# Performance work log

Measured on AMD Instinct MI355X. Metric: run time of the kernel, lower is better.

Reference implementation:

```python
import jax, jax.numpy as jnp
import numpy as np

B, F, C, H, W = 2, 16, 320, 32, 32
HEADS, DH, G = 8, 40, 32
INNER = 4 * C  # GEGLU hidden = 1280
MAXLEN = 25


def make_pe(maxlen, dm):
    pos = np.arange(maxlen)[:, None].astype(np.float64)
    div = np.exp(np.arange(0, dm, 2) * (-np.log(10000.0) / dm))
    pe = np.zeros((maxlen, dm), np.float32)
    pe[:, 0::2] = np.sin(pos * div)
    pe[:, 1::2] = np.cos(pos * div)
    return jnp.asarray(pe)

PE = make_pe(MAXLEN, C)  # [max_len, C], constant buffer


def layernorm(x, g, b, eps=1e-5):
    m = x.mean(-1, keepdims=True)
    v = jnp.var(x, axis=-1, keepdims=True)
    return (x - m) * jax.lax.rsqrt(v + eps) * g + b


def temporal_attn(hs, f, wq, wk, wv, wo, bo):
    # hs: [(b*f), d, c]; rearrange '(b f) d c -> (b d) f c'
    bf, d, c = hs.shape
    bb = bf // f
    t = hs.reshape(bb, f, d, c).transpose(0, 2, 1, 3).reshape(bb * d, f, c)
    t = t + PE[:f]  # temporal positional encoding
    def split_heads(y):
        return y.reshape(bb * d, f, HEADS, DH).transpose(0, 2, 1, 3)  # [n,h,f,dh]
    q = split_heads(t @ wq)
    k = split_heads(t @ wk)
    v = split_heads(t @ wv)
    scores = jnp.einsum('nhqd,nhkd->nhqk', q, k) * (DH ** -0.5)  # fp32
    probs = jax.nn.softmax(scores, axis=-1)
    o = jnp.einsum('nhqk,nhkd->nhqd', probs, v)
    o = o.transpose(0, 2, 1, 3).reshape(bb * d, f, c)
    o = o @ wo + bo
    # rearrange '(b d) f c -> (b f) d c'
    return o.reshape(bb, d, f, c).transpose(0, 2, 1, 3).reshape(bf, d, c)


def setup_inputs() -> dict:
    key = jax.random.key(0)
    ks = iter(jax.random.split(key, 40))
    def p(shape, s=0.02):
        return jax.random.normal(next(ks), shape, jnp.float32) * s
    inp = {"x": jax.random.normal(next(ks), (B, F, C, H, W), jnp.float32)}
    inp["gn_w"] = jnp.ones((C,), jnp.float32); inp["gn_b"] = jnp.zeros((C,), jnp.float32)
    inp["pin_w"] = p((C, C)); inp["pin_b"] = jnp.zeros((C,), jnp.float32)
    for i in (1, 2):
        inp[f"ln{i}_w"] = jnp.ones((C,), jnp.float32); inp[f"ln{i}_b"] = jnp.zeros((C,), jnp.float32)
        inp[f"wq{i}"] = p((C, C)); inp[f"wk{i}"] = p((C, C)); inp[f"wv{i}"] = p((C, C))
        inp[f"wo{i}"] = p((C, C)); inp[f"bo{i}"] = jnp.zeros((C,), jnp.float32)
    inp["ffln_w"] = jnp.ones((C,), jnp.float32); inp["ffln_b"] = jnp.zeros((C,), jnp.float32)
    inp["ff_w1"] = p((C, 2 * INNER)); inp["ff_b1"] = jnp.zeros((2 * INNER,), jnp.float32)
    inp["ff_w2"] = p((INNER, C)); inp["ff_b2"] = jnp.zeros((C,), jnp.float32)
    inp["pout_w"] = p((C, C)); inp["pout_b"] = jnp.zeros((C,), jnp.float32)
    return inp


def reference(x, gn_w, gn_b, pin_w, pin_b,
              ln1_w, ln1_b, wq1, wk1, wv1, wo1, bo1,
              ln2_w, ln2_b, wq2, wk2, wv2, wo2, bo2,
              ffln_w, ffln_b, ff_w1, ff_b1, ff_w2, ff_b2,
              pout_w, pout_b):
    b, f, c, h, w = x.shape
    xf = x.reshape(b * f, c, h, w)
    residual = xf
    # GroupNorm(32, eps=1e-6)
    xg = xf.reshape(b * f, G, c // G, h * w)
    m = xg.mean((2, 3), keepdims=True)
    v = jnp.var(xg, axis=(2, 3), keepdims=True)
    xg = (xg - m) * jax.lax.rsqrt(v + 1e-6)
    xn = xg.reshape(b * f, c, h, w) * gn_w[:, None, None] + gn_b[:, None, None]
    # to tokens + proj_in
    hs = xn.transpose(0, 2, 3, 1).reshape(b * f, h * w, c)
    hs = hs @ pin_w + pin_b
    # TemporalTransformerBlock: two temporal self-attn blocks + GEGLU FF
    hs = hs + temporal_attn(layernorm(hs, ln1_w, ln1_b), f, wq1, wk1, wv1, wo1, bo1)
    hs = hs + temporal_attn(layernorm(hs, ln2_w, ln2_b), f, wq2, wk2, wv2, wo2, bo2)
    y = layernorm(hs, ffln_w, ffln_b) @ ff_w1 + ff_b1
    a, gate = jnp.split(y, 2, axis=-1)
    hs = hs + ((a * jax.nn.gelu(gate, approximate=False)) @ ff_w2 + ff_b2)
    # proj_out + spatial residual
    hs = hs @ pout_w + pout_b
    out = hs.reshape(b * f, h, w, c).transpose(0, 3, 1, 2) + residual
    return out.reshape(b, f, c, h, w)
```

## Files before the change

### kernel.cpp

```cpp
#include <hip/hip_runtime.h>
#include <hip/hip_bf16.h>
#include <math.h>

typedef __hip_bfloat16 bf16;
typedef __attribute__((ext_vector_type(8))) short bf16x8;
typedef __attribute__((ext_vector_type(4))) float f32x4;

#define NT    32768
#define CH    320
#define NSEQ  2048
#define FRAMES 16
#define HEADS 8
#define DHEAD 40
#define INNER 1280
#define HW    1024
#define NIMG  32

__device__ __forceinline__ float b2f(bf16 v) { return __bfloat162float(v); }
__device__ __forceinline__ bf16  f2b(float v) { return __float2bfloat16(v); }
__device__ __forceinline__ float bfbits2f(unsigned short u) {
  union { unsigned int i; float f; } x; x.i = ((unsigned int)u) << 16; return x.f;
}
__device__ __forceinline__ unsigned short f2bfbits(float f) {
  union { float f; unsigned int i; } x; x.f = f;
  return (unsigned short)((x.i + 0x7FFF + ((x.i >> 16) & 1)) >> 16);
}

__device__ __forceinline__ void stage16(const bf16* g, bf16* l) {
  __builtin_amdgcn_global_load_lds(
      (const __attribute__((address_space(1))) void*)g,
      (__attribute__((address_space(3))) void*)l, 16, 0, 0);
}

__device__ __forceinline__ float block_reduce_sum(float v, float* sbuf) {
  int lane = threadIdx.x & 63;
  int wv   = threadIdx.x >> 6;
#pragma unroll
  for (int off = 32; off; off >>= 1) v += __shfl_down(v, off);
  __syncthreads();
  if (lane == 0) sbuf[wv] = v;
  __syncthreads();
  int nw = ((int)blockDim.x + 63) >> 6;
  float r = 0.f;
  for (int i = 0; i < nw; ++i) r += sbuf[i];
  return r;
}

struct TD { const float* src; bf16* dst; int K, N, t0; };
struct TDs { TD d[12]; };
__global__ __launch_bounds__(256) void transpose_w_kernel(TDs td, int ndesc) {
  __shared__ float tile[32][33];
  int bt = blockIdx.x;
  int mi = 0;
  for (int i = 1; i < 12; ++i) if (i < ndesc && bt >= td.d[i].t0) mi = i;
  TD e = td.d[mi];
  int lt = bt - e.t0;
  int ntx = e.N >> 5;
  int kt = lt / ntx, nt = lt - kt * ntx;
#pragma unroll
  for (int q = 0; q < 4; ++q) {
    int idx = threadIdx.x + q * 256; int r = idx >> 5, c = idx & 31;
    tile[r][c] = e.src[(size_t)(kt * 32 + r) * e.N + nt * 32 + c];
  }
  __syncthreads();
#pragma unroll
  for (int q = 0; q < 4; ++q) {
    int idx = threadIdx.x + q * 256; int r = idx >> 5, c = idx & 31;
    e.dst[(size_t)(nt * 32 + r) * e.K + kt * 32 + c] = f2b(tile[c][r]);
  }
}

__global__ __launch_bounds__(256) void pe_table_kernel(float* __restrict__ petab) {
  int i = blockIdx.x * 256 + threadIdx.x;
  if (i < 16 * CH) {
    int fi = i / CH, c = i - fi * CH;
    float arg = (float)fi * expf((float)(c & ~1) * -0.028782313662425575f);
    petab[i] = (c & 1) ? cosf(arg) : sinf(arg);
  }
}

__global__ __launch_bounds__(256) void ln_fused_kernel(const bf16* __restrict__ in,
                                                       const float* __restrict__ w,
                                                       const float* __restrict__ b,
                                                       bf16* __restrict__ out,
                                                       const float* __restrict__ petab,
                                                       int mode) {
  int wv = threadIdx.x >> 6, lane = threadIdx.x & 63;
  int row = blockIdx.x * 4 + wv;
  size_t base = (size_t)row * CH;
  float v[5];
  float s = 0.f;
#pragma unroll
  for (int j = 0; j < 5; ++j) {
    v[j] = b2f(in[base + lane + 64 * j]);
    s += v[j];
  }
#pragma unroll
  for (int off = 32; off; off >>= 1) s += __shfl_down(s, off);
  float mean = __shfl(s, 0) * (1.f / 320.f);
  float s2 = 0.f;
#pragma unroll
  for (int j = 0; j < 5; ++j) { float d = v[j] - mean; s2 += d * d; }
#pragma unroll
  for (int off = 32; off; off >>= 1) s2 += __shfl_down(s2, off);
  float rstd = rsqrtf(__shfl(s2, 0) * (1.f / 320.f) + 1e-5f);
  size_t obase = base;
  const float* pe = nullptr;
  if (mode) {
    int img = row >> 10, dd = row & 1023, bb = img >> 4, fi = img & 15;
    int trow = (((bb << 10) + dd) << 4) + fi;
    obase = (size_t)trow * CH;
    pe = petab + fi * CH;
  }
#pragma unroll
  for (int j = 0; j < 5; ++j) {
    int c = lane + 64 * j;
    float o = (v[j] - mean) * rstd * w[c] + b[c];
    if (mode) o += pe[c];
    out[obase + c] = f2b(o);
  }
}

__global__ __launch_bounds__(256) void gemm_mfma_kernel(
    const bf16* __restrict__ A, const bf16* __restrict__ BT,
    const float* __restrict__ bias, const bf16* res,
    bf16* C0, bf16* C1, bf16* C2, int M, int K, int rowmap) {
  __shared__ __align__(16) bf16 sA[128 * 64];
  __shared__ __align__(16) bf16 sB[64 * 64];
  int tid = threadIdx.x, lane = tid & 63, w = tid >> 6;
  int wm = w >> 1, wn = w & 1;
  int m0 = blockIdx.x * 128, n0 = blockIdx.y * 64;
  int which = n0 / 320;
  int ncol0 = n0 - which * 320;
  bf16* C = which == 0 ? C0 : (which == 1 ? C1 : C2);
  f32x4 acc[4][2];
#pragma unroll
  for (int i = 0; i < 4; ++i)
#pragma unroll
    for (int j = 0; j < 2; ++j) acc[i][j] = (f32x4){0.f, 0.f, 0.f, 0.f};

  int lr = lane >> 3;
  int cg = (lane & 7) ^ lr;
  for (int k0 = 0; k0 < K; k0 += 64) {
#pragma unroll
    for (int s = 0; s < 4; ++s) {
      int tA = w * 4 + s;
      int row = tA * 8 + lr;
      stage16(A + (size_t)(m0 + row) * K + k0 + cg * 8, sA + tA * 512);
    }
#pragma unroll
    for (int s = 0; s < 2; ++s) {
      int tB = w * 2 + s;
      int row = tB * 8 + lr;
      stage16(BT + (size_t)(n0 + row) * K + k0 + cg * 8, sB + tB * 512);
    }
    __syncthreads();
#pragma unroll
    for (int kk = 0; kk < 2; ++kk) {
      bf16x8 a[4], b[2];
      int cc = kk * 4 + (lane >> 4);
#pragma unroll
      for (int i = 0; i < 4; ++i) {
        int r = wm * 64 + i * 16 + (lane & 15);
        a[i] = *(const bf16x8*)(sA + r * 64 + ((cc ^ (r & 7)) * 8));
      }
#pragma unroll
      for (int j = 0; j < 2; ++j) {
        int n = wn * 32 + j * 16 + (lane & 15);
        b[j] = *(const bf16x8*)(sB + n * 64 + ((cc ^ (n & 7)) * 8));
      }
#pragma unroll
      for (int i = 0; i < 4; ++i)
#pragma unroll
        for (int j = 0; j < 2; ++j)
          acc[i][j] = __builtin_amdgcn_mfma_f32_16x16x32_bf16(a[i], b[j], acc[i][j], 0, 0, 0);
    }
    __syncthreads();
  }
#pragma unroll
  for (int i = 0; i < 4; ++i)
#pragma unroll
    for (int j = 0; j < 2; ++j) {
      int row0 = m0 + wm * 64 + i * 16 + (lane >> 4) * 4;
      int col  = ncol0 + wn * 32 + j * 16 + (lane & 15);
      float bv = bias ? bias[col] : 0.f;
#pragma unroll
      for (int rg = 0; rg < 4; ++rg) {
        int r = row0 + rg;
        if (rowmap) {
          int n = r >> 4, fi = r & 15, bb = n >> 10, dd = n & 1023;
          r = ((bb << 4) + fi) * 1024 + dd;
        }
        size_t idx = (size_t)r * 320 + col;
        float v = acc[i][j][rg] + bv;
        if (res) v += b2f(res[idx]);
        C[idx] = f2b(v);
      }
    }
}

__global__ __launch_bounds__(256) void gemm_mfma_geglu_kernel(
    const bf16* __restrict__ A, const bf16* __restrict__ BT,
    const float* __restrict__ b1, bf16* __restrict__ act, int M, int K) {
  __shared__ __align__(16) bf16 sA[128 * 64];
  __shared__ __align__(16) bf16 sBa[64 * 64];
  __shared__ __align__(16) bf16 sBg[64 * 64];
  int tid = threadIdx.x, lane = tid & 63, w = tid >> 6;
  int wm = w >> 1, wn = w & 1;
  int m0 = blockIdx.x * 128, n0 = blockIdx.y * 64;
  f32x4 aa[4][2], ag[4][2];
#pragma unroll
  for (int i = 0; i < 4; ++i)
#pragma unroll
    for (int j = 0; j < 2; ++j) {
      aa[i][j] = (f32x4){0.f, 0.f, 0.f, 0.f};
      ag[i][j] = (f32x4){0.f, 0.f, 0.f, 0.f};
    }
  int lr = lane >> 3;
  int cg = (lane & 7) ^ lr;
  for (int k0 = 0; k0 < K; k0 += 64) {
#pragma unroll
    for (int s = 0; s < 4; ++s) {
      int tA = w * 4 + s;
      int row = tA * 8 + lr;
      stage16(A + (size_t)(m0 + row) * K + k0 + cg * 8, sA + tA * 512);
    }
#pragma unroll
    for (int s = 0; s < 2; ++s) {
      int tB = w * 2 + s;
      int row = tB * 8 + lr;
      stage16(BT + (size_t)(n0 + row) * K + k0 + cg * 8, sBa + tB * 512);
      stage16(BT + (size_t)(1280 + n0 + row) * K + k0 + cg * 8, sBg + tB * 512);
    }
    __syncthreads();
#pragma unroll
    for (int kk = 0; kk < 2; ++kk) {
      bf16x8 a[4], ba[2], bg[2];
      int cc = kk * 4 + (lane >> 4);
#pragma unroll
      for (int i = 0; i < 4; ++i) {
        int r = wm * 64 + i * 16 + (lane & 15);
        a[i] = *(const bf16x8*)(sA + r * 64 + ((cc ^ (r & 7)) * 8));
      }
#pragma unroll
      for (int j = 0; j < 2; ++j) {
        int n = wn * 32 + j * 16 + (lane & 15);
        ba[j] = *(const bf16x8*)(sBa + n * 64 + ((cc ^ (n & 7)) * 8));
        bg[j] = *(const bf16x8*)(sBg + n * 64 + ((cc ^ (n & 7)) * 8));
      }
#pragma unroll
      for (int i = 0; i < 4; ++i)
#pragma unroll
        for (int j = 0; j < 2; ++j) {
          aa[i][j] = __builtin_amdgcn_mfma_f32_16x16x32_bf16(a[i], ba[j], aa[i][j], 0, 0, 0);
          ag[i][j] = __builtin_amdgcn_mfma_f32_16x16x32_bf16(a[i], bg[j], ag[i][j], 0, 0, 0);
        }
    }
    __syncthreads();
  }
#pragma unroll
  for (int i = 0; i < 4; ++i)
#pragma unroll
    for (int j = 0; j < 2; ++j) {
      int row0 = m0 + wm * 64 + i * 16 + (lane >> 4) * 4;
      int col  = n0 + wn * 32 + j * 16 + (lane & 15);
      float bva = b1[col], bvg = b1[1280 + col];
#pragma unroll
      for (int rg = 0; rg < 4; ++rg) {
        float av = aa[i][j][rg] + bva;
        float gv = ag[i][j][rg] + bvg;
        float gelu = 0.5f * gv * (1.0f + erff(gv * 0.70710678118654752f));
        act[(size_t)(row0 + rg) * 1280 + col] = f2b(av * gelu);
      }
    }
}

__global__ __launch_bounds__(256) void gn_stats_kernel(const float* __restrict__ x,
                                                       float* __restrict__ stat) {
  __shared__ float sbuf[8];
  int g  = blockIdx.x;
  int im = blockIdx.y;
  const float* base = x + ((size_t)im * CH + (size_t)g * 10) * HW;
  float s = 0.f, s2 = 0.f;
  for (int i = threadIdx.x; i < 10 * HW; i += 256) {
    float v = base[i];
    s += v; s2 += v * v;
  }
  s  = block_reduce_sum(s, sbuf);
  s2 = block_reduce_sum(s2, sbuf);
  if (threadIdx.x == 0) {
    float mean = s * (1.f / 10240.f);
    float var  = s2 * (1.f / 10240.f) - mean * mean;
    stat[(im * 32 + g) * 2 + 0] = mean;
    stat[(im * 32 + g) * 2 + 1] = rsqrtf(var + 1e-6f);
  }
}

__global__ __launch_bounds__(256) void gn_apply_kernel(const float* __restrict__ x,
                                                       const float* __restrict__ gw,
                                                       const float* __restrict__ gb,
                                                       const float* __restrict__ stat,
                                                       bf16* __restrict__ xn) {
  __shared__ float tile[32][33];
  int st = blockIdx.x, ct = blockIdx.y, im = blockIdx.z;
  int c0 = ct * 32, s0 = st * 32;
  for (int t = threadIdx.x; t < 1024; t += 256) {
    int i = t >> 5, j = t & 31;
    int c = c0 + i;
    int g = c / 10;
    float mean = stat[(im * 32 + g) * 2 + 0];
    float rstd = stat[(im * 32 + g) * 2 + 1];
    tile[i][j] = (x[((size_t)(im * CH + c) << 10) + s0 + j] - mean) * rstd * gw[c] + gb[c];
  }
  __syncthreads();
  for (int t = threadIdx.x; t < 1024; t += 256) {
    int i = t >> 5, j = t & 31;
    xn[((size_t)(im * HW + s0 + i)) * CH + c0 + j] = f2b(tile[j][i]);
  }
}

#define AROW 324
__global__ __launch_bounds__(256) void attention_kernel(const bf16* __restrict__ Q,
                                                        const bf16* __restrict__ K,
                                                        const bf16* __restrict__ V,
                                                        bf16* __restrict__ O) {
  __shared__ float q[16 * AROW];
  __shared__ float k[16 * AROW];
  __shared__ float v[16 * AROW];
  __shared__ float sc[HEADS * 16 * 16];
  const float SCALE = 0.15811388300841897f;
  int tid = threadIdx.x;
  int n = blockIdx.x;
  size_t base = (size_t)n * FRAMES * CH;
  for (int j = tid; j < 1280; j += 256) {
    int row = j / 80, off = (j - row * 80) * 4;
    int src = row * 320 + off;
    ushort4 uq = *(const ushort4*)(Q + base + src);
    ushort4 uk = *(const ushort4*)(K + base + src);
    ushort4 uv = *(const ushort4*)(V + base + src);
    float* qd = &q[row * AROW + off];
    float* kd = &k[row * AROW + off];
    float* vd = &v[row * AROW + off];
    qd[0] = bfbits2f(uq.x) * SCALE; qd[1] = bfbits2f(uq.y) * SCALE;
    qd[2] = bfbits2f(uq.z) * SCALE; qd[3] = bfbits2f(uq.w) * SCALE;
    kd[0] = bfbits2f(uk.x); kd[1] = bfbits2f(uk.y);
    kd[2] = bfbits2f(uk.z); kd[3] = bfbits2f(uk.w);
    vd[0] = bfbits2f(uv.x); vd[1] = bfbits2f(uv.y);
    vd[2] = bfbits2f(uv.z); vd[3] = bfbits2f(uv.w);
  }
  __syncthreads();
  {
    int h = tid >> 5, sub = tid & 31, qf = sub >> 1, kfg = sub & 1;
    const float* qrow = &q[qf * AROW + h * DHEAD];
    float s[8] = {0.f, 0.f, 0.f, 0.f, 0.f, 0.f, 0.f, 0.f};
#pragma unroll
    for (int d4 = 0; d4 < 10; ++d4) {
      float4 qv = *(const float4*)(qrow + d4 * 4);
#pragma unroll
      for (int i = 0; i < 8; ++i) {
        const float* krow = &k[(kfg * 8 + i) * AROW + h * DHEAD];
        float4 kv = *(const float4*)(krow + d4 * 4);
        s[i] += qv.x * kv.x + qv.y * kv.y + qv.z * kv.z + qv.w * kv.w;
      }
    }
    float* dst = &sc[(h * 16 + qf) * 16 + kfg * 8];
#pragma unroll
    for (int i = 0; i < 8; ++i) dst[i] = s[i];
  }
  __syncthreads();
  if (tid < 128) {
    float* r = &sc[tid * 16];
    float mx = r[0];
#pragma unroll
    for (int i = 1; i < 16; ++i) mx = fmaxf(mx, r[i]);
    float sum = 0.f;
#pragma unroll
    for (int i = 0; i < 16; ++i) { float e = expf(r[i] - mx); r[i] = e; sum += e; }
    float inv = 1.0f / sum;
#pragma unroll
    for (int i = 0; i < 16; ++i) r[i] *= inv;
  }
  __syncthreads();
  for (int g = tid; g < 1280; g += 256) {
    int qf = g / 80, c4 = g - qf * 80;
    int h = c4 / 10;
    const float* p = &sc[(h * 16 + qf) * 16];
    float4 o = {0.f, 0.f, 0.f, 0.f};
#pragma unroll
    for (int kf = 0; kf < 16; ++kf) {
      float pv = p[kf];
      float4 vv = *(const float4*)&v[kf * AROW + c4 * 4];
      o.x += pv * vv.x; o.y += pv * vv.y; o.z += pv * vv.z; o.w += pv * vv.w;
    }
    ushort4 u;
    u.x = f2bfbits(o.x); u.y = f2bfbits(o.y);
    u.z = f2bfbits(o.z); u.w = f2bfbits(o.w);
    *(ushort4*)(O + base + qf * 320 + c4 * 4) = u;
  }
}

__global__ __launch_bounds__(256) void final_kernel(const bf16* __restrict__ proj,
                                                    const float* __restrict__ x,
                                                    float* __restrict__ out) {
  __shared__ float tile[32][33];
  int st = blockIdx.x, ct = blockIdx.y, im = blockIdx.z;
  int c0 = ct * 32, s0 = st * 32;
  for (int t = threadIdx.x; t < 1024; t += 256) {
    int i = t >> 5, j = t & 31;
    tile[i][j] = b2f(proj[((size_t)(im * HW + s0 + i)) * CH + c0 + j]);
  }
  __syncthreads();
  for (int t = threadIdx.x; t < 1024; t += 256) {
    int i = t >> 5, j = t & 31;
    size_t idx = ((size_t)(im * CH + c0 + i) << 10) + s0 + j;
    out[idx] = tile[j][i] + x[idx];
  }
}

extern "C" void kernel_launch(void* const* d_in, const int* in_sizes, int n_in,
                              void* d_out, int out_size, void* d_ws, size_t ws_size,
                              hipStream_t stream) {
  const float* x      = (const float*)d_in[0];
  const float* gn_w   = (const float*)d_in[1];
  const float* gn_b   = (const float*)d_in[2];
  const float* pin_w  = (const float*)d_in[3];
  const float* pin_b  = (const float*)d_in[4];
  const float* ffln_w = (const float*)d_in[19];
  const float* ffln_b = (const float*)d_in[20];
  const float* ff_w1  = (const float*)d_in[21];
  const float* ff_b1  = (const float*)d_in[22];
  const float* ff_w2  = (const float*)d_in[23];
  const float* ff_b2  = (const float*)d_in[24];
  const float* pout_w = (const float*)d_in[25];
  const float* pout_b = (const float*)d_in[26];

  const size_t NTC = (size_t)NT * CH;
  bf16* W0 = (bf16*)d_ws;
  bf16* W1 = W0 + NTC;
  bf16* W2 = W1 + NTC;
  bf16* W3 = W2 + NTC;
  bf16* OB = (bf16*)d_out;
  float* gnstat = (float*)d_out;
  bf16* WT = (bf16*)d_out + NTC;
  bf16* wt_pin  = WT;
  bf16* wt_qkv1 = wt_pin + 102400;
  bf16* wt_wo1  = wt_qkv1 + 307200;
  bf16* wt_qkv2 = wt_wo1 + 102400;
  bf16* wt_wo2  = wt_qkv2 + 307200;
  bf16* wt_ff1  = wt_wo2 + 102400;
  bf16* wt_ff2  = wt_ff1 + 819200;
  bf16* wt_pout = wt_ff2 + 409600;
  float* petab  = (float*)(wt_pout + 102400);

  TDs td; int t0 = 0;
  auto add = [&](int i, const float* s, bf16* d, int K, int N) {
    td.d[i] = {s, d, K, N, t0}; t0 += (K / 32) * (N / 32);
  };
  add(0, pin_w, wt_pin, 320, 320);
  add(1, (const float*)d_in[7],  wt_qkv1,          320, 320);
  add(2, (const float*)d_in[8],  wt_qkv1 + 102400, 320, 320);
  add(3, (const float*)d_in[9],  wt_qkv1 + 204800, 320, 320);
  add(4, (const float*)d_in[10], wt_wo1,           320, 320);
  add(5, (const float*)d_in[14], wt_qkv2,          320, 320);
  add(6, (const float*)d_in[15], wt_qkv2 + 102400, 320, 320);
  add(7, (const float*)d_in[16], wt_qkv2 + 204800, 320, 320);
  add(8, (const float*)d_in[17], wt_wo2,           320, 320);
  add(9, ff_w1, wt_ff1, 320, 2560);
  add(10, ff_w2, wt_ff2, 1280, 320);
  add(11, pout_w, wt_pout, 320, 320);
  transpose_w_kernel<<<t0, 256, 0, stream>>>(td, 12);
  pe_table_kernel<<<20, 256, 0, stream>>>(petab);

  dim3 g_trans(32, 10, NIMG);
  dim3 g_gemm(NT / 128, 5);

  gn_stats_kernel<<<dim3(32, NIMG), 256, 0, stream>>>(x, gnstat);
  gn_apply_kernel<<<g_trans, 256, 0, stream>>>(x, gn_w, gn_b, gnstat, W1);
  gemm_mfma_kernel<<<g_gemm, 256, 0, stream>>>(W1, wt_pin, pin_b, nullptr,
                                               W0, W0, W0, NT, CH, 0);

  for (int blk = 0; blk < 2; ++blk) {
    const float* lnw = (const float*)d_in[5 + 7 * blk];
    const float* lnb = (const float*)d_in[6 + 7 * blk];
    const float* bo  = (const float*)d_in[11 + 7 * blk];
    bf16* wt_qkv = blk ? wt_qkv2 : wt_qkv1;
    bf16* wt_wo  = blk ? wt_wo2  : wt_wo1;

    ln_fused_kernel<<<NT / 4, 256, 0, stream>>>(W0, lnw, lnb, W2, petab, 1);
    gemm_mfma_kernel<<<dim3(NT / 128, 15), 256, 0, stream>>>(W2, wt_qkv, nullptr, nullptr,
                                                             W3, OB, W1, NT, CH, 0);
    attention_kernel<<<NSEQ, 256, 0, stream>>>(W3, OB, W1, W2);
    gemm_mfma_kernel<<<g_gemm, 256, 0, stream>>>(W2, wt_wo, bo, W0,
                                                 W0, W0, W0, NT, CH, 1);
  }

  ln_fused_kernel<<<NT / 4, 256, 0, stream>>>(W0, ffln_w, ffln_b, W1, nullptr, 0);
  const int MH = NT / 2;
  for (int h = 0; h < 2; ++h) {
    const bf16* Ah = W1 + (size_t)h * MH * CH;
    bf16* act = W2;
    gemm_mfma_geglu_kernel<<<dim3(MH / 128, 20), 256, 0, stream>>>(Ah, wt_ff1, ff_b1,
                                                                   act, MH, CH);
    bf16* hsh = W0 + (size_t)h * MH * CH;
    gemm_mfma_kernel<<<dim3(MH / 128, 5), 256, 0, stream>>>(act, wt_ff2, ff_b2, hsh,
                                                            hsh, hsh, hsh, MH, INNER, 0);
  }

  gemm_mfma_kernel<<<g_gemm, 256, 0, stream>>>(W0, wt_pout, pout_b, nullptr,
                                               W1, W1, W1, NT, CH, 0);
  final_kernel<<<g_trans, 256, 0, stream>>>(W1, x, (float*)d_out);
}
```

Measured before the change: 595.7 us.

## Widen GEMM N-tiles and fuse proj_out with transpose and residual epilogue

The generic MFMA GEMM now uses 128x160 tiles instead of 128x64, and the GEGLU GEMM uses 128x128 tiles per gate/value half, so each block reuses A tiles across more columns and the grid shrinks. The proj_out GEMM gets a new rowmap==2 epilogue that writes fp32 output directly in channel-major layout and adds the input residual, which removes the separate final transpose kernel and its bf16 intermediate. The pout weight transpose moves to just before that GEMM, into a free workspace buffer. In exchange, accumulator register and LDS use per block rise, which may lower occupancy, and the fused store writes float4 along the spatial axis from MFMA row groups.

```diff
diff --git a/kernel.cpp b/kernel.cpp
--- a/kernel.cpp
+++ b/kernel.cpp
@@ -124,20 +124,22 @@
 __global__ __launch_bounds__(256) void gemm_mfma_kernel(
     const bf16* __restrict__ A, const bf16* __restrict__ BT,
     const float* __restrict__ bias, const bf16* res,
-    bf16* C0, bf16* C1, bf16* C2, int M, int K, int rowmap) {
+    bf16* C0, bf16* C1, bf16* C2,
+    const float* __restrict__ resF, float* __restrict__ outF,
+    int M, int K, int rowmap) {
   __shared__ __align__(16) bf16 sA[128 * 64];
-  __shared__ __align__(16) bf16 sB[64 * 64];
+  __shared__ __align__(16) bf16 sB[160 * 64];
   int tid = threadIdx.x, lane = tid & 63, w = tid >> 6;
   int wm = w >> 1, wn = w & 1;
-  int m0 = blockIdx.x * 128, n0 = blockIdx.y * 64;
+  int m0 = blockIdx.x * 128, n0 = blockIdx.y * 160;
   int which = n0 / 320;
   int ncol0 = n0 - which * 320;
   bf16* C = which == 0 ? C0 : (which == 1 ? C1 : C2);
-  f32x4 acc[4][2];
+  f32x4 acc[4][5];
 #pragma unroll
   for (int i = 0; i < 4; ++i)
 #pragma unroll
-    for (int j = 0; j < 2; ++j) acc[i][j] = (f32x4){0.f, 0.f, 0.f, 0.f};
+    for (int j = 0; j < 5; ++j) acc[i][j] = (f32x4){0.f, 0.f, 0.f, 0.f};
 
   int lr = lane >> 3;
   int cg = (lane & 7) ^ lr;
@@ -149,15 +151,15 @@
       stage16(A + (size_t)(m0 + row) * K + k0 + cg * 8, sA + tA * 512);
     }
 #pragma unroll
-    for (int s = 0; s < 2; ++s) {
-      int tB = w * 2 + s;
+    for (int s = 0; s < 5; ++s) {
+      int tB = w * 5 + s;
       int row = tB * 8 + lr;
       stage16(BT + (size_t)(n0 + row) * K + k0 + cg * 8, sB + tB * 512);
     }
     __syncthreads();
 #pragma unroll
     for (int kk = 0; kk < 2; ++kk) {
-      bf16x8 a[4], b[2];
+      bf16x8 a[4], b[5];
       int cc = kk * 4 + (lane >> 4);
 #pragma unroll
       for (int i = 0; i < 4; ++i) {
@@ -165,14 +167,14 @@
         a[i] = *(const bf16x8*)(sA + r * 64 + ((cc ^ (r & 7)) * 8));
       }
 #pragma unroll
-      for (int j = 0; j < 2; ++j) {
-        int n = wn * 32 + j * 16 + (lane & 15);
+      for (int j = 0; j < 5; ++j) {
+        int n = wn * 80 + j * 16 + (lane & 15);
         b[j] = *(const bf16x8*)(sB + n * 64 + ((cc ^ (n & 7)) * 8));
       }
 #pragma unroll
       for (int i = 0; i < 4; ++i)
 #pragma unroll
-        for (int j = 0; j < 2; ++j)
+        for (int j = 0; j < 5; ++j)
           acc[i][j] = __builtin_amdgcn_mfma_f32_16x16x32_bf16(a[i], b[j], acc[i][j], 0, 0, 0);
     }
     __syncthreads();
@@ -180,21 +182,33 @@
 #pragma unroll
   for (int i = 0; i < 4; ++i)
 #pragma unroll
-    for (int j = 0; j < 2; ++j) {
+    for (int j = 0; j < 5; ++j) {
       int row0 = m0 + wm * 64 + i * 16 + (lane >> 4) * 4;
-      int col  = ncol0 + wn * 32 + j * 16 + (lane & 15);
+      int col  = ncol0 + wn * 80 + j * 16 + (lane & 15);
       float bv = bias ? bias[col] : 0.f;
-#pragma unroll
-      for (int rg = 0; rg < 4; ++rg) {
-        int r = row0 + rg;
-        if (rowmap) {
-          int n = r >> 4, fi = r & 15, bb = n >> 10, dd = n & 1023;
-          r = ((bb << 4) + fi) * 1024 + dd;
+      if (rowmap == 2) {
+        int im = row0 >> 10, s0r = row0 & 1023;
+        size_t oidx = ((size_t)(im * 320 + col) << 10) + s0r;
+        float4 xr = *(const float4*)(resF + oidx);
+        float4 ov;
+        ov.x = acc[i][j][0] + bv + xr.x;
+        ov.y = acc[i][j][1] + bv + xr.y;
+        ov.z = acc[i][j][2] + bv + xr.z;
+        ov.w = acc[i][j][3] + bv + xr.w;
+        *(float4*)(outF + oidx) = ov;
+      } else {
+#pragma unroll
+        for (int rg = 0; rg < 4; ++rg) {
+          int r = row0 + rg;
+          if (rowmap == 1) {
+            int n = r >> 4, fi = r & 15, bb = n >> 10, dd = n & 1023;
+            r = ((bb << 4) + fi) * 1024 + dd;
+          }
+          size_t idx = (size_t)r * 320 + col;
+          float v = acc[i][j][rg] + bv;
+          if (res) v += b2f(res[idx]);
+          C[idx] = f2b(v);
         }
-        size_t idx = (size_t)r * 320 + col;
-        float v = acc[i][j][rg] + bv;
-        if (res) v += b2f(res[idx]);
-        C[idx] = f2b(v);
       }
     }
 }
@@ -203,16 +217,16 @@
     const bf16* __restrict__ A, const bf16* __restrict__ BT,
     const float* __restrict__ b1, bf16* __restrict__ act, int M, int K) {
   __shared__ __align__(16) bf16 sA[128 * 64];
-  __shared__ __align__(16) bf16 sBa[64 * 64];
-  __shared__ __align__(16) bf16 sBg[64 * 64];
+  __shared__ __align__(16) bf16 sBa[128 * 64];
+  __shared__ __align__(16) bf16 sBg[128 * 64];
   int tid = threadIdx.x, lane = tid & 63, w = tid >> 6;
   int wm = w >> 1, wn = w & 1;
-  int m0 = blockIdx.x * 128, n0 = blockIdx.y * 64;
-  f32x4 aa[4][2], ag[4][2];
+  int m0 = blockIdx.x * 128, n0 = blockIdx.y * 128;
+  f32x4 aa[4][4], ag[4][4];
 #pragma unroll
   for (int i = 0; i < 4; ++i)
 #pragma unroll
-    for (int j = 0; j < 2; ++j) {
+    for (int j = 0; j < 4; ++j) {
       aa[i][j] = (f32x4){0.f, 0.f, 0.f, 0.f};
       ag[i][j] = (f32x4){0.f, 0.f, 0.f, 0.f};
     }
@@ -226,8 +240,8 @@
       stage16(A + (size_t)(m0 + row) * K + k0 + cg * 8, sA + tA * 512);
     }
 #pragma unroll
-    for (int s = 0; s < 2; ++s) {
-      int tB = w * 2 + s;
+    for (int s = 0; s < 4; ++s) {
+      int tB = w * 4 + s;
       int row = tB * 8 + lr;
       stage16(BT + (size_t)(n0 + row) * K + k0 + cg * 8, sBa + tB * 512);
       stage16(BT + (size_t)(1280 + n0 + row) * K + k0 + cg * 8, sBg + tB * 512);
@@ -235,7 +249,7 @@
     __syncthreads();
 #pragma unroll
     for (int kk = 0; kk < 2; ++kk) {
-      bf16x8 a[4], ba[2], bg[2];
+      bf16x8 a[4], ba[4], bg[4];
       int cc = kk * 4 + (lane >> 4);
 #pragma unroll
       for (int i = 0; i < 4; ++i) {
@@ -243,15 +257,15 @@
         a[i] = *(const bf16x8*)(sA + r * 64 + ((cc ^ (r & 7)) * 8));
       }
 #pragma unroll
-      for (int j = 0; j < 2; ++j) {
-        int n = wn * 32 + j * 16 + (lane & 15);
+      for (int j = 0; j < 4; ++j) {
+        int n = wn * 64 + j * 16 + (lane & 15);
         ba[j] = *(const bf16x8*)(sBa + n * 64 + ((cc ^ (n & 7)) * 8));
         bg[j] = *(const bf16x8*)(sBg + n * 64 + ((cc ^ (n & 7)) * 8));
       }
 #pragma unroll
       for (int i = 0; i < 4; ++i)
 #pragma unroll
-        for (int j = 0; j < 2; ++j) {
+        for (int j = 0; j < 4; ++j) {
           aa[i][j] = __builtin_amdgcn_mfma_f32_16x16x32_bf16(a[i], ba[j], aa[i][j], 0, 0, 0);
           ag[i][j] = __builtin_amdgcn_mfma_f32_16x16x32_bf16(a[i], bg[j], ag[i][j], 0, 0, 0);
         }
@@ -261,9 +275,9 @@
 #pragma unroll
   for (int i = 0; i < 4; ++i)
 #pragma unroll
-    for (int j = 0; j < 2; ++j) {
+    for (int j = 0; j < 4; ++j) {
       int row0 = m0 + wm * 64 + i * 16 + (lane >> 4) * 4;
-      int col  = n0 + wn * 32 + j * 16 + (lane & 15);
+      int col  = n0 + wn * 64 + j * 16 + (lane & 15);
       float bva = b1[col], bvg = b1[1280 + col];
 #pragma unroll
       for (int rg = 0; rg < 4; ++rg) {
@@ -399,24 +413,6 @@
   }
 }
 
-__global__ __launch_bounds__(256) void final_kernel(const bf16* __restrict__ proj,
-                                                    const float* __restrict__ x,
-                                                    float* __restrict__ out) {
-  __shared__ float tile[32][33];
-  int st = blockIdx.x, ct = blockIdx.y, im = blockIdx.z;
-  int c0 = ct * 32, s0 = st * 32;
-  for (int t = threadIdx.x; t < 1024; t += 256) {
-    int i = t >> 5, j = t & 31;
-    tile[i][j] = b2f(proj[((size_t)(im * HW + s0 + i)) * CH + c0 + j]);
-  }
-  __syncthreads();
-  for (int t = threadIdx.x; t < 1024; t += 256) {
-    int i = t >> 5, j = t & 31;
-    size_t idx = ((size_t)(im * CH + c0 + i) << 10) + s0 + j;
-    out[idx] = tile[j][i] + x[idx];
-  }
-}
-
 extern "C" void kernel_launch(void* const* d_in, const int* in_sizes, int n_in,
                               void* d_out, int out_size, void* d_ws, size_t ws_size,
                               hipStream_t stream) {
@@ -449,8 +445,7 @@
   bf16* wt_wo2  = wt_qkv2 + 307200;
   bf16* wt_ff1  = wt_wo2 + 102400;
   bf16* wt_ff2  = wt_ff1 + 819200;
-  bf16* wt_pout = wt_ff2 + 409600;
-  float* petab  = (float*)(wt_pout + 102400);
+  float* petab  = (float*)(wt_ff2 + 409600);
 
   TDs td; int t0 = 0;
   auto add = [&](int i, const float* s, bf16* d, int K, int N) {
@@ -467,17 +462,17 @@
   add(8, (const float*)d_in[17], wt_wo2,           320, 320);
   add(9, ff_w1, wt_ff1, 320, 2560);
   add(10, ff_w2, wt_ff2, 1280, 320);
-  add(11, pout_w, wt_pout, 320, 320);
-  transpose_w_kernel<<<t0, 256, 0, stream>>>(td, 12);
+  td.d[11] = td.d[0];
+  transpose_w_kernel<<<t0, 256, 0, stream>>>(td, 11);
   pe_table_kernel<<<20, 256, 0, stream>>>(petab);
 
   dim3 g_trans(32, 10, NIMG);
-  dim3 g_gemm(NT / 128, 5);
+  dim3 g_gemm(NT / 128, 2);
 
   gn_stats_kernel<<<dim3(32, NIMG), 256, 0, stream>>>(x, gnstat);
   gn_apply_kernel<<<g_trans, 256, 0, stream>>>(x, gn_w, gn_b, gnstat, W1);
   gemm_mfma_kernel<<<g_gemm, 256, 0, stream>>>(W1, wt_pin, pin_b, nullptr,
-                                               W0, W0, W0, NT, CH, 0);
+                                               W0, W0, W0, nullptr, nullptr, NT, CH, 0);
 
   for (int blk = 0; blk < 2; ++blk) {
     const float* lnw = (const float*)d_in[5 + 7 * blk];
@@ -487,11 +482,11 @@
     bf16* wt_wo  = blk ? wt_wo2  : wt_wo1;
 
     ln_fused_kernel<<<NT / 4, 256, 0, stream>>>(W0, lnw, lnb, W2, petab, 1);
-    gemm_mfma_kernel<<<dim3(NT / 128, 15), 256, 0, stream>>>(W2, wt_qkv, nullptr, nullptr,
-                                                             W3, OB, W1, NT, CH, 0);
+    gemm_mfma_kernel<<<dim3(NT / 128, 6), 256, 0, stream>>>(W2, wt_qkv, nullptr, nullptr,
+                                                            W3, OB, W1, nullptr, nullptr, NT, CH, 0);
     attention_kernel<<<NSEQ, 256, 0, stream>>>(W3, OB, W1, W2);
     gemm_mfma_kernel<<<g_gemm, 256, 0, stream>>>(W2, wt_wo, bo, W0,
-                                                 W0, W0, W0, NT, CH, 1);
+                                                 W0, W0, W0, nullptr, nullptr, NT, CH, 1);
   }
 
   ln_fused_kernel<<<NT / 4, 256, 0, stream>>>(W0, ffln_w, ffln_b, W1, nullptr, 0);
@@ -499,14 +494,18 @@
   for (int h = 0; h < 2; ++h) {
     const bf16* Ah = W1 + (size_t)h * MH * CH;
     bf16* act = W2;
-    gemm_mfma_geglu_kernel<<<dim3(MH / 128, 20), 256, 0, stream>>>(Ah, wt_ff1, ff_b1,
+    gemm_mfma_geglu_kernel<<<dim3(MH / 128, 10), 256, 0, stream>>>(Ah, wt_ff1, ff_b1,
                                                                    act, MH, CH);
     bf16* hsh = W0 + (size_t)h * MH * CH;
-    gemm_mfma_kernel<<<dim3(MH / 128, 5), 256, 0, stream>>>(act, wt_ff2, ff_b2, hsh,
-                                                            hsh, hsh, hsh, MH, INNER, 0);
-  }
-
-  gemm_mfma_kernel<<<g_gemm, 256, 0, stream>>>(W0, wt_pout, pout_b, nullptr,
-                                               W1, W1, W1, NT, CH, 0);
-  final_kernel<<<g_trans, 256, 0, stream>>>(W1, x, (float*)d_out);
-}
+    gemm_mfma_kernel<<<dim3(MH / 128, 2), 256, 0, stream>>>(act, wt_ff2, ff_b2, hsh,
+                                                            hsh, hsh, hsh, nullptr, nullptr,
+                                                            MH, INNER, 0);
+  }
+
+  TDs tdp; tdp.d[0] = {pout_w, W1, 320, 320, 0};
+  for (int i = 1; i < 12; ++i) tdp.d[i] = tdp.d[0];
+  transpose_w_kernel<<<100, 256, 0, stream>>>(tdp, 1);
+  gemm_mfma_kernel<<<g_gemm, 256, 0, stream>>>(W0, W1, pout_b, nullptr,
+                                               nullptr, nullptr, nullptr,
+                                               x, (float*)d_out, NT, CH, 2);
+}
```

After: 759.1 us. 1.27x slower.
